# Kernel tuning notes

Measured on AMD Instinct MI355X. Metric: run time of the kernel, lower is better.

Reference implementation:

```python
import jax, jax.numpy as jnp
import numpy as np

D_MODEL = 1024
N_HEADS = 16
D_KV = 64
B, S = 2, 2048


def setup_inputs() -> dict:
    key = jax.random.key(0)
    ks = jax.random.split(key, 7)
    scale = 1.0 / np.sqrt(D_MODEL)
    return {
        "query": jax.random.normal(ks[0], (B, S, D_MODEL), jnp.float32),
        "key": jax.random.normal(ks[1], (B, S, D_MODEL), jnp.float32),
        "value": jax.random.normal(ks[2], (B, S, D_MODEL), jnp.float32),
        "mask": jnp.zeros((B, 1, 1, S), jnp.float32),
        "Wq": jax.random.normal(ks[3], (D_MODEL, N_HEADS * D_KV), jnp.float32) * scale,
        "Wk": jax.random.normal(ks[4], (D_MODEL, N_HEADS * D_KV), jnp.float32) * scale,
        "Wv": jax.random.normal(ks[5], (D_MODEL, N_HEADS * D_KV), jnp.float32) * scale,
        "Wo": jax.random.normal(ks[6], (N_HEADS * D_KV, D_MODEL), jnp.float32) * scale,
    }


def _split_heads(x):
    b, s, _ = x.shape
    return x.reshape(b, s, N_HEADS, D_KV).transpose(0, 2, 1, 3)  # [B,H,S,Dk]


def reference(query, key, value, mask, Wq, Wk, Wv, Wo):
    q = _split_heads(query @ Wq)
    k = _split_heads(key @ Wk)
    v = _split_heads(value @ Wv)
    scores = jnp.einsum("bhqd,bhkd->bhqk", q, k) / jnp.sqrt(
        jnp.asarray(D_KV, scores_dtype := q.dtype)
    )
    scores = scores + mask
    attn = jax.nn.softmax(scores, axis=-1)  # dropout_rate=0 -> identity
    ctx = jnp.einsum("bhqk,bhkd->bhqd", attn, v)
    ctx = ctx.transpose(0, 2, 1, 3).reshape(query.shape[0], -1, N_HEADS * D_KV)
    hidden = ctx @ Wo
    return hidden
```

## Files before the change

kernel.cpp:

```cpp
#include <hip/hip_runtime.h>
#include <hip/hip_bf16.h>
#include <stdint.h>

typedef __bf16 bf16;
typedef __bf16 bf16x8 __attribute__((ext_vector_type(8)));
typedef __bf16 bf16x4 __attribute__((ext_vector_type(4)));
typedef float  f32x4  __attribute__((ext_vector_type(4)));
typedef float  f32x16 __attribute__((ext_vector_type(16)));

#define S_LEN  2048
#define NH     16
#define DKV    64
#define DMODEL 1024
#define LOG2E  1.4426950408889634f

__device__ __forceinline__ void async_load16(const void* g, void* l) {
  __builtin_amdgcn_global_load_lds(
      (const __attribute__((address_space(1))) uint32_t*)(uintptr_t)g,
      (__attribute__((address_space(3))) uint32_t*)(uintptr_t)l,
      16, 0, 0);
}

__global__ void transpose_w(const float* __restrict__ W0, const float* __restrict__ W1,
                            const float* __restrict__ W2, const float* __restrict__ W3,
                            bf16* __restrict__ T0, bf16* __restrict__ T1,
                            bf16* __restrict__ T2, bf16* __restrict__ T3)
{
  int z = blockIdx.z;
  const float* W = (z == 0) ? W0 : (z == 1) ? W1 : (z == 2) ? W2 : W3;
  bf16* T = (z == 0) ? T0 : (z == 1) ? T1 : (z == 2) ? T2 : T3;
  __shared__ float tile[32][33];
  int n0 = blockIdx.x * 32, k0 = blockIdx.y * 32;
  int tx = threadIdx.x, ty = threadIdx.y;
  for (int i = 0; i < 32; i += 8)
    tile[ty + i][tx] = W[(size_t)(k0 + ty + i) * DMODEL + n0 + tx];
  __syncthreads();
  for (int i = 0; i < 32; i += 8)
    T[(size_t)(n0 + ty + i) * DMODEL + k0 + tx] = (bf16)tile[tx][ty + i];
}

__global__ __launch_bounds__(256) void gemm_qkv(
    const float* __restrict__ Aq, const float* __restrict__ Ak, const float* __restrict__ Av,
    const bf16* __restrict__ Bq, const bf16* __restrict__ Bk, const bf16* __restrict__ Bv,
    bf16* __restrict__ Cq, bf16* __restrict__ Ck, bf16* __restrict__ Cv)
{
  __shared__ __align__(16) char smem[24576];
  bf16* As = (bf16*)smem;
  bf16* Bs = (bf16*)smem + 64 * 64;
  bf16* Ls = (bf16*)smem;

  const int z = blockIdx.z;
  const float* A = (z == 0) ? Aq : (z == 1) ? Ak : Av;
  const bf16* Bt = (z == 0) ? Bq : (z == 1) ? Bk : Bv;
  bf16* C        = (z == 0) ? Cq : (z == 1) ? Ck : Cv;

  const int m0 = blockIdx.x * 64;
  const int n0 = blockIdx.y * 128;
  const int tid = threadIdx.x;
  const int lane = tid & 63;
  const int wave = tid >> 6;
  const int wm = (wave >> 1) * 32;
  const int wn = (wave & 1) * 64;
  const int row = lane & 15;
  const int quad = lane >> 4;

  f32x4 acc[2][4];
  for (int i = 0; i < 2; ++i)
    for (int j = 0; j < 4; ++j) acc[i][j] = (f32x4){0.f, 0.f, 0.f, 0.f};

  const int arc = tid & 7;
  const int arr = tid >> 3;

  for (int kt = 0; kt < 16; ++kt) {
    const int kk = kt << 6;
    f32x4 av0[2], av1[2];
    for (int u = 0; u < 2; ++u) {
      const float* sp = A + (size_t)(m0 + u * 32 + arr) * DMODEL + kk + arc * 8;
      av0[u] = *(const f32x4*)sp;
      av1[u] = *(const f32x4*)(sp + 4);
    }
    __syncthreads();
    for (int j = 0; j < 4; ++j) {
      int base = j * 256 + wave * 64;
      int idx = base + lane;
      int r = idx >> 3;
      int cc = (idx & 7) ^ (r & 7);
      async_load16(Bt + (size_t)(n0 + r) * DMODEL + kk + cc * 8,
                   (char*)Bs + (size_t)base * 16);
    }
    for (int u = 0; u < 2; ++u) {
      bf16x8 o;
      for (int w = 0; w < 4; ++w) { o[w] = (bf16)av0[u][w]; o[w + 4] = (bf16)av1[u][w]; }
      int r = u * 32 + arr;
      *(bf16x8*)(As + r * 64 + ((arc ^ (r & 7)) << 3)) = o;
    }
    __syncthreads();
    for (int ks = 0; ks < 2; ++ks) {
      bf16x8 af[2], bfr[4];
      for (int i = 0; i < 2; ++i) {
        int rr = wm + i * 16 + row;
        af[i] = *(const bf16x8*)(As + rr * 64 + (((quad + ks * 4) ^ (rr & 7)) << 3));
      }
      for (int j = 0; j < 4; ++j) {
        int rr = wn + j * 16 + row;
        bfr[j] = *(const bf16x8*)(Bs + rr * 64 + (((quad + ks * 4) ^ (rr & 7)) << 3));
      }
      for (int i = 0; i < 2; ++i)
        for (int j = 0; j < 4; ++j)
          acc[i][j] = __builtin_amdgcn_mfma_f32_16x16x32_bf16(af[i], bfr[j], acc[i][j], 0, 0, 0);
    }
  }

  if (z != 2) {
    const int bq = m0 >> 11;
    __syncthreads();
    for (int i = 0; i < 2; ++i)
      for (int j = 0; j < 4; ++j)
        for (int r = 0; r < 4; ++r)
          Ls[(wm + i * 16 + quad * 4 + r) * 132 + wn + j * 16 + row] = (bf16)acc[i][j][r];
    __syncthreads();
    for (int u = 0; u < 4; ++u) {
      int cc = u * 256 + tid;
      int rloc = cc >> 4, c8 = (cc & 15) * 8;
      int s = (m0 + rloc) & 2047;
      int gn = n0 + c8;
      int h = gn >> 6, d = gn & 63;
      bf16x8 val = *(const bf16x8*)(Ls + rloc * 132 + c8);
      *(bf16x8*)(C + (((size_t)(bq * NH + h)) * S_LEN + s) * DKV + d) = val;
    }
  } else {
    for (int i = 0; i < 2; ++i)
      for (int j = 0; j < 4; ++j) {
        int gm = m0 + wm + i * 16 + quad * 4;
        int gn = n0 + wn + j * 16 + row;
        int b = gm >> 11, s = gm & 2047;
        int h = gn >> 6,  d = gn & 63;
        int bh = b * NH + h;
        int tile = s >> 6, kb = (s & 63) >> 2;
        bf16x4 t;
        for (int r = 0; r < 4; ++r) t[r] = (bf16)acc[i][j][r];
        *(bf16x4*)(C + ((((size_t)bh * 32 + tile) * 16 + kb) * 64 + d) * 4) = t;
      }
  }
}

__global__ __launch_bounds__(256, 4) void attn_kernel(
    const bf16* __restrict__ Qh, const bf16* __restrict__ Kh, const bf16* __restrict__ Vperm,
    const float* __restrict__ mask, bf16* __restrict__ Opart, float* __restrict__ Lpart)
{
  __shared__ __align__(16) bf16 Ks[64 * 64];
  __shared__ __align__(16) bf16 Vts[64 * 64];
  __shared__ __align__(16) float masks2[64];

  const int bh = blockIdx.x;
  const int b = bh >> 4;
  const int q0 = blockIdx.y * 128;
  const int zh = blockIdx.z;
  const int tid = threadIdx.x;
  const int lane = tid & 63;
  const int wave = tid >> 6;
  const int ln = lane & 31;
  const int hi = lane >> 5;
  const float SC2 = 0.125f * LOG2E;

  const int qg = q0 + wave * 32 + ln;
  bf16x8 qf[4];
  {
    const bf16* qrow = Qh + ((size_t)bh * S_LEN + qg) * DKV;
    for (int c = 0; c < 4; ++c)
      qf[c] = *(const bf16x8*)(qrow + c * 16 + hi * 8);
  }

  f32x16 O[2];
  for (int nb = 0; nb < 2; ++nb)
    for (int i = 0; i < 16; ++i) O[nb][i] = 0.f;
  float lsum = 0.f;

  for (int it = 0; it < 16; ++it) {
    const int kv0 = zh * 1024 + it * 64;
    __syncthreads();
    const bf16* vtile = Vperm + ((size_t)bh * 32 + (kv0 >> 6)) * 4096;
    for (int j = 0; j < 2; ++j) {
      int base = j * 256 + wave * 64;
      int idx = base + lane;
      int r = idx >> 3;
      int cc = (idx & 7) ^ (r & 7);
      async_load16(Kh + ((size_t)bh * S_LEN + kv0 + r) * DKV + cc * 8,
                   (char*)Ks + (size_t)base * 16);
      async_load16(vtile + (size_t)idx * 8,
                   (char*)Vts + (size_t)base * 16);
    }
    if (tid < 64) masks2[tid] = mask[b * S_LEN + kv0 + tid] * LOG2E;
    __syncthreads();

    f32x16 Sm[2];
    for (int i = 0; i < 16; ++i) { Sm[0][i] = 0.f; Sm[1][i] = 0.f; }
    for (int c = 0; c < 4; ++c) {
      bf16x8 k0 = *(const bf16x8*)(Ks + ln * 64        + (((2 * c + hi) ^ (ln & 7)) << 3));
      bf16x8 k1 = *(const bf16x8*)(Ks + (32 + ln) * 64 + (((2 * c + hi) ^ (ln & 7)) << 3));
      Sm[0] = __builtin_amdgcn_mfma_f32_32x32x16_bf16(k0, qf[c], Sm[0], 0, 0, 0);
      Sm[1] = __builtin_amdgcn_mfma_f32_32x32x16_bf16(k1, qf[c], Sm[1], 0, 0, 0);
    }

    for (int cg = 0; cg < 4; ++cg) {
      int mb = cg >> 1, g = cg & 1;
      int koff = 32 * mb + 16 * g + 4 * hi;
      f32x4 mklo = *(const f32x4*)(masks2 + koff);
      f32x4 mkhi = *(const f32x4*)(masks2 + koff + 8);
      bf16x8 ap;
      float ls0 = 0.f;
      for (int u = 0; u < 4; ++u) {
        float p = __builtin_amdgcn_exp2f(Sm[mb][g * 8 + u] * SC2 + mklo[u]);
        ls0 += p; ap[u] = (bf16)p;
      }
      for (int u = 0; u < 4; ++u) {
        float p = __builtin_amdgcn_exp2f(Sm[mb][g * 8 + 4 + u] * SC2 + mkhi[u]);
        ls0 += p; ap[4 + u] = (bf16)p;
      }
      lsum += ls0;
      int kb0 = hi + 4 * g + 8 * mb;
      for (int nb = 0; nb < 2; ++nb) {
        int d = nb * 32 + ln;
        bf16x4 lo = *(const bf16x4*)(Vts + ((size_t)kb0 * 64 + d) * 4);
        bf16x4 hv = *(const bf16x4*)(Vts + ((size_t)(kb0 + 2) * 64 + d) * 4);
        bf16x8 bv;
        for (int u = 0; u < 4; ++u) { bv[u] = lo[u]; bv[u + 4] = hv[u]; }
        O[nb] = __builtin_amdgcn_mfma_f32_32x32x16_bf16(ap, bv, O[nb], 0, 0, 0);
      }
    }
  }

  float lt = lsum + __shfl_xor(lsum, 32, 64);
  if (lane < 32)
    Lpart[((size_t)zh * 32 + bh) * S_LEN + q0 + wave * 32 + ln] = lt;

  bf16* ob = Opart + (((size_t)zh * 32 + bh) * S_LEN) * DKV;
  for (int g = 0; g < 4; ++g)
    for (int nb = 0; nb < 2; ++nb)
      for (int j = 0; j < 4; ++j) {
        int qrow = q0 + wave * 32 + j + 8 * g + 4 * hi;
        ob[(size_t)qrow * DKV + nb * 32 + ln] = (bf16)O[nb][g * 4 + j];
      }
}

__global__ __launch_bounds__(256) void gemm_out(
    const bf16* __restrict__ Opart, const float* __restrict__ Lpart,
    const bf16* __restrict__ Wot, float* __restrict__ Cout)
{
  __shared__ __align__(16) bf16 As[32 * 64];
  __shared__ __align__(16) bf16 Bs[128 * 64];
  __shared__ float rinv[NH * 32];

  const int m0 = blockIdx.x * 32;
  const int n0 = blockIdx.y * 128;
  const int tid = threadIdx.x;
  const int lane = tid & 63;
  const int wave = tid >> 6;
  const int wm = (wave >> 1) * 16;
  const int wn = (wave & 1) * 64;
  const int row = lane & 15;
  const int quad = lane >> 4;
  const int b = m0 >> 11;
  const int s0 = m0 & 2047;

  for (int u = 0; u < 2; ++u) {
    int idx = u * 256 + tid;
    int h = idx >> 5, r = idx & 31;
    float l = Lpart[((size_t)(b * NH + h)) * S_LEN + s0 + r]
            + Lpart[((size_t)(32 + b * NH + h)) * S_LEN + s0 + r];
    rinv[idx] = 1.0f / l;
  }

  f32x4 acc[4];
  for (int j = 0; j < 4; ++j) acc[j] = (f32x4){0.f, 0.f, 0.f, 0.f};

  const int arc = tid & 7;
  const int arr = tid >> 3;

  for (int kt = 0; kt < 16; ++kt) {
    bf16x8 h0 = *(const bf16x8*)(Opart + ((size_t)(b * NH + kt) * S_LEN + s0 + arr) * DKV + arc * 8);
    bf16x8 h1 = *(const bf16x8*)(Opart + ((size_t)(32 + b * NH + kt) * S_LEN + s0 + arr) * DKV + arc * 8);
    __syncthreads();
    for (int j = 0; j < 4; ++j) {
      int base = j * 256 + wave * 64;
      int idx = base + lane;
      int r = idx >> 3;
      int cc = (idx & 7) ^ (r & 7);
      async_load16(Wot + (size_t)(n0 + r) * DMODEL + kt * 64 + cc * 8,
                   (char*)Bs + (size_t)base * 16);
    }
    {
      float rv = rinv[kt * 32 + arr];
      bf16x8 o;
      for (int w = 0; w < 8; ++w)
        o[w] = (bf16)(((float)h0[w] + (float)h1[w]) * rv);
      *(bf16x8*)(As + arr * 64 + ((arc ^ (arr & 7)) << 3)) = o;
    }
    __syncthreads();
    for (int ks = 0; ks < 2; ++ks) {
      bf16x8 af, bfr[4];
      {
        int rr = wm + row;
        af = *(const bf16x8*)(As + rr * 64 + (((quad + ks * 4) ^ (rr & 7)) << 3));
      }
      for (int j = 0; j < 4; ++j) {
        int rr = wn + j * 16 + row;
        bfr[j] = *(const bf16x8*)(Bs + rr * 64 + (((quad + ks * 4) ^ (rr & 7)) << 3));
      }
      for (int j = 0; j < 4; ++j)
        acc[j] = __builtin_amdgcn_mfma_f32_16x16x32_bf16(af, bfr[j], acc[j], 0, 0, 0);
    }
  }

  for (int j = 0; j < 4; ++j)
    for (int r = 0; r < 4; ++r) {
      int gm = m0 + wm + quad * 4 + r;
      int gn = n0 + wn + j * 16 + row;
      Cout[(size_t)gm * DMODEL + gn] = acc[j][r];
    }
}

extern "C" void kernel_launch(void* const* d_in, const int* in_sizes, int n_in,
                              void* d_out, int out_size, void* d_ws, size_t ws_size,
                              hipStream_t stream)
{
  const float* query = (const float*)d_in[0];
  const float* key_  = (const float*)d_in[1];
  const float* value = (const float*)d_in[2];
  const float* mask  = (const float*)d_in[3];
  const float* Wq = (const float*)d_in[4];
  const float* Wk = (const float*)d_in[5];
  const float* Wv = (const float*)d_in[6];
  const float* Wo = (const float*)d_in[7];

  char* ws = (char*)d_ws;
  const size_t MB = (size_t)1 << 20;
  bf16* qh    = (bf16*)(ws + 0 * MB);
  bf16* kh    = (bf16*)(ws + 8 * MB);
  bf16* vperm = (bf16*)(ws + 16 * MB);
  bf16* wot   = (bf16*)(ws + 24 * MB);
  bf16* Opart = (bf16*)(ws + 26 * MB);
  bf16* wqt   = (bf16*)(ws + 26 * MB);
  bf16* wkt   = (bf16*)(ws + 28 * MB);
  bf16* wvt   = (bf16*)(ws + 30 * MB);
  float* Lpart = (float*)(ws + 58 * MB);

  transpose_w<<<dim3(32, 32, 4), dim3(32, 8), 0, stream>>>(Wq, Wk, Wv, Wo, wqt, wkt, wvt, wot);
  gemm_qkv<<<dim3(64, 8, 3), 256, 0, stream>>>(query, key_, value, wqt, wkt, wvt,
                                               qh, kh, vperm);
  attn_kernel<<<dim3(32, 16, 2), 256, 0, stream>>>(qh, kh, vperm, mask, Opart, Lpart);
  gemm_out<<<dim3(128, 8), 256, 0, stream>>>(Opart, Lpart, wot, (float*)d_out);
}
```

Measured before the change: 217.2 us.

## Double-buffer LDS tiles in QKV and output projection GEMMs

Both projection GEMMs now use two LDS buffers, with register prefetch two k-steps ahead. The next tile's weight DMA and activation conversion are issued before the MFMA work on the current tile, so only one barrier per iteration remains. The aim is to hide global-load latency behind matrix math. In exchange, the QKV GEMM's LDS grows to 48KB and there is more register pressure, which may lower occupancy.

```diff
diff --git a/kernel.cpp b/kernel.cpp
--- a/kernel.cpp
+++ b/kernel.cpp
@@ -44,10 +44,10 @@
     const bf16* __restrict__ Bq, const bf16* __restrict__ Bk, const bf16* __restrict__ Bv,
     bf16* __restrict__ Cq, bf16* __restrict__ Ck, bf16* __restrict__ Cv)
 {
-  __shared__ __align__(16) char smem[24576];
-  bf16* As = (bf16*)smem;
-  bf16* Bs = (bf16*)smem + 64 * 64;
-  bf16* Ls = (bf16*)smem;
+  __shared__ __align__(16) char smem[49152];
+  bf16* As0 = (bf16*)smem;
+  bf16* Bs0 = (bf16*)smem + 2 * 64 * 64;
+  bf16* Ls  = (bf16*)smem;
 
   const int z = blockIdx.z;
   const float* A = (z == 0) ? Aq : (z == 1) ? Ak : Av;
@@ -70,50 +70,69 @@
 
   const int arc = tid & 7;
   const int arr = tid >> 3;
+  const float* A0p = A + (size_t)(m0 + arr) * DMODEL + arc * 8;
+  const float* A1p = A + (size_t)(m0 + 32 + arr) * DMODEL + arc * 8;
+
+  f32x4 av0[2], av1[2];
+  #define LOAD_A(kt) {                                   \
+    const int kn_ = (kt) << 6;                           \
+    av0[0] = *(const f32x4*)(A0p + kn_);                 \
+    av1[0] = *(const f32x4*)(A0p + kn_ + 4);             \
+    av0[1] = *(const f32x4*)(A1p + kn_);                 \
+    av1[1] = *(const f32x4*)(A1p + kn_ + 4);             \
+  }
+  #define CVT_A(p) {                                     \
+    bf16* Ab_ = As0 + (p) * 4096;                        \
+    for (int u = 0; u < 2; ++u) {                        \
+      bf16x8 o;                                          \
+      for (int w = 0; w < 4; ++w) { o[w] = (bf16)av0[u][w]; o[w + 4] = (bf16)av1[u][w]; } \
+      int r_ = u * 32 + arr;                             \
+      *(bf16x8*)(Ab_ + r_ * 64 + ((arc ^ (r_ & 7)) << 3)) = o; \
+    }                                                    \
+  }
+  #define DMA_B(kt, p) {                                 \
+    const int kk_ = (kt) << 6;                           \
+    for (int j = 0; j < 4; ++j) {                        \
+      int base_ = j * 256 + wave * 64;                   \
+      int idx_ = base_ + lane;                           \
+      int r_ = idx_ >> 3;                                \
+      int cc_ = (idx_ & 7) ^ (r_ & 7);                   \
+      async_load16(Bt + (size_t)(n0 + r_) * DMODEL + kk_ + cc_ * 8, \
+                   (char*)(Bs0 + (p) * 8192) + (size_t)base_ * 16); \
+    }                                                    \
+  }
+
+  LOAD_A(0);
+  DMA_B(0, 0);
+  CVT_A(0);
+  LOAD_A(1);
+  __syncthreads();
 
   for (int kt = 0; kt < 16; ++kt) {
-    const int kk = kt << 6;
-    f32x4 av0[2], av1[2];
-    for (int u = 0; u < 2; ++u) {
-      const float* sp = A + (size_t)(m0 + u * 32 + arr) * DMODEL + kk + arc * 8;
-      av0[u] = *(const f32x4*)sp;
-      av1[u] = *(const f32x4*)(sp + 4);
-    }
-    __syncthreads();
-    for (int j = 0; j < 4; ++j) {
-      int base = j * 256 + wave * 64;
-      int idx = base + lane;
-      int r = idx >> 3;
-      int cc = (idx & 7) ^ (r & 7);
-      async_load16(Bt + (size_t)(n0 + r) * DMODEL + kk + cc * 8,
-                   (char*)Bs + (size_t)base * 16);
-    }
-    for (int u = 0; u < 2; ++u) {
-      bf16x8 o;
-      for (int w = 0; w < 4; ++w) { o[w] = (bf16)av0[u][w]; o[w + 4] = (bf16)av1[u][w]; }
-      int r = u * 32 + arr;
-      *(bf16x8*)(As + r * 64 + ((arc ^ (r & 7)) << 3)) = o;
-    }
-    __syncthreads();
+    const int p = kt & 1;
+    if (kt < 15) { DMA_B(kt + 1, p ^ 1); CVT_A(p ^ 1); }
+    if (kt < 14) LOAD_A(kt + 2);
+    const bf16* Ab = As0 + p * 4096;
+    const bf16* Bb = Bs0 + p * 8192;
     for (int ks = 0; ks < 2; ++ks) {
       bf16x8 af[2], bfr[4];
       for (int i = 0; i < 2; ++i) {
         int rr = wm + i * 16 + row;
-        af[i] = *(const bf16x8*)(As + rr * 64 + (((quad + ks * 4) ^ (rr & 7)) << 3));
+        af[i] = *(const bf16x8*)(Ab + rr * 64 + (((quad + ks * 4) ^ (rr & 7)) << 3));
       }
       for (int j = 0; j < 4; ++j) {
         int rr = wn + j * 16 + row;
-        bfr[j] = *(const bf16x8*)(Bs + rr * 64 + (((quad + ks * 4) ^ (rr & 7)) << 3));
+        bfr[j] = *(const bf16x8*)(Bb + rr * 64 + (((quad + ks * 4) ^ (rr & 7)) << 3));
       }
       for (int i = 0; i < 2; ++i)
         for (int j = 0; j < 4; ++j)
           acc[i][j] = __builtin_amdgcn_mfma_f32_16x16x32_bf16(af[i], bfr[j], acc[i][j], 0, 0, 0);
     }
+    __syncthreads();
   }
 
   if (z != 2) {
     const int bq = m0 >> 11;
-    __syncthreads();
     for (int i = 0; i < 2; ++i)
       for (int j = 0; j < 4; ++j)
         for (int r = 0; r < 4; ++r)
@@ -142,6 +161,9 @@
         *(bf16x4*)(C + ((((size_t)bh * 32 + tile) * 16 + kb) * 64 + d) * 4) = t;
       }
   }
+  #undef LOAD_A
+  #undef CVT_A
+  #undef DMA_B
 }
 
 __global__ __launch_bounds__(256, 4) void attn_kernel(
@@ -247,8 +269,8 @@
     const bf16* __restrict__ Opart, const float* __restrict__ Lpart,
     const bf16* __restrict__ Wot, float* __restrict__ Cout)
 {
-  __shared__ __align__(16) bf16 As[32 * 64];
-  __shared__ __align__(16) bf16 Bs[128 * 64];
+  __shared__ __align__(16) bf16 As0[2][32 * 64];
+  __shared__ __align__(16) bf16 Bs0[2][128 * 64];
   __shared__ float rinv[NH * 32];
 
   const int m0 = blockIdx.x * 32;
@@ -270,46 +292,66 @@
             + Lpart[((size_t)(32 + b * NH + h)) * S_LEN + s0 + r];
     rinv[idx] = 1.0f / l;
   }
+  __syncthreads();
 
   f32x4 acc[4];
   for (int j = 0; j < 4; ++j) acc[j] = (f32x4){0.f, 0.f, 0.f, 0.f};
 
   const int arc = tid & 7;
   const int arr = tid >> 3;
+  const bf16* O0p = Opart + ((size_t)(b * NH) * S_LEN + s0 + arr) * DKV + arc * 8;
+  const bf16* O1p = Opart + ((size_t)(32 + b * NH) * S_LEN + s0 + arr) * DKV + arc * 8;
+  const size_t HSTEP = (size_t)S_LEN * DKV;
+
+  bf16x8 h0, h1;
+  #define LOAD_O(kt) {                                   \
+    h0 = *(const bf16x8*)(O0p + (size_t)(kt) * HSTEP);   \
+    h1 = *(const bf16x8*)(O1p + (size_t)(kt) * HSTEP);   \
+  }
+  #define CVT_O(kt, p) {                                 \
+    float rv_ = rinv[(kt) * 32 + arr];                   \
+    bf16x8 o_;                                           \
+    for (int w = 0; w < 8; ++w)                          \
+      o_[w] = (bf16)(((float)h0[w] + (float)h1[w]) * rv_); \
+    *(bf16x8*)(&As0[p][0] + arr * 64 + ((arc ^ (arr & 7)) << 3)) = o_; \
+  }
+  #define DMA_W(kt, p) {                                 \
+    for (int j = 0; j < 4; ++j) {                        \
+      int base_ = j * 256 + wave * 64;                   \
+      int idx_ = base_ + lane;                           \
+      int r_ = idx_ >> 3;                                \
+      int cc_ = (idx_ & 7) ^ (r_ & 7);                   \
+      async_load16(Wot + (size_t)(n0 + r_) * DMODEL + (kt) * 64 + cc_ * 8, \
+                   (char*)(&Bs0[p][0]) + (size_t)base_ * 16); \
+    }                                                    \
+  }
+
+  LOAD_O(0);
+  DMA_W(0, 0);
+  CVT_O(0, 0);
+  LOAD_O(1);
+  __syncthreads();
 
   for (int kt = 0; kt < 16; ++kt) {
-    bf16x8 h0 = *(const bf16x8*)(Opart + ((size_t)(b * NH + kt) * S_LEN + s0 + arr) * DKV + arc * 8);
-    bf16x8 h1 = *(const bf16x8*)(Opart + ((size_t)(32 + b * NH + kt) * S_LEN + s0 + arr) * DKV + arc * 8);
-    __syncthreads();
-    for (int j = 0; j < 4; ++j) {
-      int base = j * 256 + wave * 64;
-      int idx = base + lane;
-      int r = idx >> 3;
-      int cc = (idx & 7) ^ (r & 7);
-      async_load16(Wot + (size_t)(n0 + r) * DMODEL + kt * 64 + cc * 8,
-                   (char*)Bs + (size_t)base * 16);
-    }
-    {
-      float rv = rinv[kt * 32 + arr];
-      bf16x8 o;
-      for (int w = 0; w < 8; ++w)
-        o[w] = (bf16)(((float)h0[w] + (float)h1[w]) * rv);
-      *(bf16x8*)(As + arr * 64 + ((arc ^ (arr & 7)) << 3)) = o;
-    }
-    __syncthreads();
+    const int p = kt & 1;
+    if (kt < 15) { DMA_W(kt + 1, p ^ 1); CVT_O(kt + 1, p ^ 1); }
+    if (kt < 14) LOAD_O(kt + 2);
+    const bf16* Ab = &As0[p][0];
+    const bf16* Bb = &Bs0[p][0];
     for (int ks = 0; ks < 2; ++ks) {
       bf16x8 af, bfr[4];
       {
         int rr = wm + row;
-        af = *(const bf16x8*)(As + rr * 64 + (((quad + ks * 4) ^ (rr & 7)) << 3));
+        af = *(const bf16x8*)(Ab + rr * 64 + (((quad + ks * 4) ^ (rr & 7)) << 3));
       }
       for (int j = 0; j < 4; ++j) {
         int rr = wn + j * 16 + row;
-        bfr[j] = *(const bf16x8*)(Bs + rr * 64 + (((quad + ks * 4) ^ (rr & 7)) << 3));
+        bfr[j] = *(const bf16x8*)(Bb + rr * 64 + (((quad + ks * 4) ^ (rr & 7)) << 3));
       }
       for (int j = 0; j < 4; ++j)
         acc[j] = __builtin_amdgcn_mfma_f32_16x16x32_bf16(af, bfr[j], acc[j], 0, 0, 0);
     }
+    __syncthreads();
   }
 
   for (int j = 0; j < 4; ++j)
@@ -318,6 +360,9 @@
       int gn = n0 + wn + j * 16 + row;
       Cout[(size_t)gm * DMODEL + gn] = acc[j][r];
     }
+  #undef LOAD_O
+  #undef CVT_O
+  #undef DMA_W
 }
 
 extern "C" void kernel_launch(void* const* d_in, const int* in_sizes, int n_in,
```

Result: slower. 234.0 us (+7.7%).
